# Performance work log

Hardware: AMD Instinct MI355X
Metric: run time of the kernel (lower is better)

The kernel has to match this reference:

```python
import jax, jax.numpy as jnp
import numpy as np

NH, NL, NP_ = 8, 4, 4  # heads, levels, sampling points per head per level
SPATIAL_SHAPES = [(128, 128), (64, 64), (32, 32), (16, 16)]  # (H, W) per level
LIN = sum(h * w for h, w in SPATIAL_SHAPES)  # 21760


def _layernorm(x, g, b, eps=1e-5):
    m = x.mean(-1, keepdims=True)
    v = ((x - m) ** 2).mean(-1, keepdims=True)
    return (x - m) * jax.lax.rsqrt(v + eps) * g + b


def _sample_level(v, H, W, loc):
    # v: [B, NH, H*W, DH] level feature map; loc: [B, Lq, NH, NP, 2] in [0,1]
    # torch grid_sample semantics: align_corners=False, padding_mode='zeros'
    x = loc[..., 0] * W - 0.5
    y = loc[..., 1] * H - 0.5
    x0 = jnp.floor(x); y0 = jnp.floor(y)
    wx = x - x0; wy = y - y0
    x0i = x0.astype(jnp.int32); y0i = y0.astype(jnp.int32)

    def gat(xi, yi):
        valid = (xi >= 0) & (xi < W) & (yi >= 0) & (yi < H)
        idx = jnp.clip(yi, 0, H - 1) * W + jnp.clip(xi, 0, W - 1)  # [B,Lq,NH,NP]
        B_, Lq, nh, P = idx.shape
        idx_t = idx.transpose(0, 2, 1, 3).reshape(B_, nh, Lq * P)
        g = jnp.take_along_axis(v, idx_t[..., None], axis=2)  # [B,NH,Lq*P,DH]
        g = g.reshape(B_, nh, Lq, P, -1).transpose(0, 2, 1, 3, 4)  # [B,Lq,NH,P,DH]
        return g * valid[..., None]

    return (gat(x0i, y0i) * ((1 - wx) * (1 - wy))[..., None]
            + gat(x0i + 1, y0i) * (wx * (1 - wy))[..., None]
            + gat(x0i, y0i + 1) * ((1 - wx) * wy)[..., None]
            + gat(x0i + 1, y0i + 1) * (wx * wy)[..., None])


def _msda(query, ref, src, off_w, off_b, attw_w, attw_b, val_w, val_b, mout_w, mout_b):
    B, Lq, C = query.shape
    DH = C // NH
    value = (src @ val_w.T + val_b).reshape(B, -1, NH, DH).transpose(0, 2, 1, 3)  # [B,NH,Lin,DH]
    offs = (query @ off_w.T + off_b).reshape(B, Lq, NH, NL, NP_, 2)
    aw = jax.nn.softmax((query @ attw_w.T + attw_b).reshape(B, Lq, NH, NL * NP_), axis=-1)
    aw = aw.reshape(B, Lq, NH, NL, NP_)
    # offset normalizer is (W, H) per level
    norm = jnp.array([[w, h] for (h, w) in SPATIAL_SHAPES], jnp.float32)
    loc = ref[:, :, None, :, None, :] + offs / norm[None, None, None, :, None, :]
    out = jnp.zeros((B, Lq, NH, DH), query.dtype)
    start = 0
    for l, (H, W) in enumerate(SPATIAL_SHAPES):
        v_l = value[:, :, start:start + H * W, :]
        start += H * W
        s = _sample_level(v_l, H, W, loc[:, :, :, l])  # [B,Lq,NH,NP,DH]
        out = out + jnp.einsum('bqhpd,bqhp->bqhd', s, aw[:, :, :, l, :])
    return out.reshape(B, Lq, C) @ mout_w.T + mout_b


def _forward(tgt, query_pos, reference_points, src,
             inproj_w, inproj_b, outproj_w, outproj_b,
             ln_inter_g, ln_inter_b, ln_cross_g, ln_cross_b, ln3_g, ln3_b,
             off_w, off_b, attw_w, attw_b, val_w, val_b, mout_w, mout_b,
             lin1_w, lin1_b, lin2_w, lin2_b):
    B, Q, P, C = tgt.shape
    DH = C // NH
    # ---- inter (self) attention over instance axis Q, batched over B*P ----
    x = tgt.swapaxes(1, 2).reshape(B * P, Q, C)
    qkv = x @ inproj_w.T + inproj_b
    q, k, v = jnp.split(qkv, 3, axis=-1)
    q = q.reshape(B * P, Q, NH, DH)
    k = k.reshape(B * P, Q, NH, DH)
    v = v.reshape(B * P, Q, NH, DH)
    att = jax.nn.softmax(jnp.einsum('nqhd,nkhd->nhqk', q, k) / np.float32(np.sqrt(DH)), axis=-1)
    o = jnp.einsum('nhqk,nkhd->nqhd', att, v).reshape(B * P, Q, C) @ outproj_w.T + outproj_b
    x = _layernorm((x + o).reshape(B, P, Q, C), ln_inter_g, ln_inter_b).swapaxes(1, 2)  # [B,Q,P,C]
    # ---- multi-scale deformable cross-attention ----
    query = (x + query_pos).reshape(B, Q * P, C)
    ref = reference_points.reshape(B, Q * P, NL, 2)
    t2 = _msda(query, ref, src, off_w, off_b, attw_w, attw_b, val_w, val_b, mout_w, mout_b).reshape(B, Q, P, C)
    x = _layernorm(x + t2, ln_cross_g, ln_cross_b)
    # ---- FFN ----
    h = jax.nn.relu(x @ lin1_w.T + lin1_b)
    return _layernorm(x + h @ lin2_w.T + lin2_b, ln3_g, ln3_b)


def setup_inputs() -> dict:
    key = jax.random.key(0)
    ks = jax.random.split(key, 24)
    B, Q, P, C, DFF = 4, 300, 16, 256, 1024
    f = jax.random.normal
    w = lambda k, shape: f(k, shape, jnp.float32) * 0.02
    starts = np.cumsum([0] + [h * ww for h, ww in SPATIAL_SHAPES])[:-1]
    return {
        'tgt': f(ks[0], (B, Q, P, C), jnp.float32),
        'query_pos': f(ks[1], (B, Q, P, C), jnp.float32) * 0.1,
        'reference_points': jax.random.uniform(ks[2], (B, Q, P, NL, 2), jnp.float32),
        'src': f(ks[3], (B, LIN, C), jnp.float32),
        'src_spatial_shapes': jnp.array(SPATIAL_SHAPES, jnp.int32),
        'level_start_index': jnp.array(starts, jnp.int32),
        'inproj_w': w(ks[4], (3 * C, C)), 'inproj_b': jnp.zeros((3 * C,), jnp.float32),
        'outproj_w': w(ks[5], (C, C)), 'outproj_b': jnp.zeros((C,), jnp.float32),
        'ln_inter_g': jnp.ones((C,), jnp.float32), 'ln_inter_b': jnp.zeros((C,), jnp.float32),
        'ln_cross_g': jnp.ones((C,), jnp.float32), 'ln_cross_b': jnp.zeros((C,), jnp.float32),
        'ln3_g': jnp.ones((C,), jnp.float32), 'ln3_b': jnp.zeros((C,), jnp.float32),
        'off_w': w(ks[6], (NH * NL * NP_ * 2, C)), 'off_b': jnp.zeros((NH * NL * NP_ * 2,), jnp.float32),
        'attw_w': w(ks[7], (NH * NL * NP_, C)), 'attw_b': jnp.zeros((NH * NL * NP_,), jnp.float32),
        'val_w': w(ks[8], (C, C)), 'val_b': jnp.zeros((C,), jnp.float32),
        'mout_w': w(ks[9], (C, C)), 'mout_b': jnp.zeros((C,), jnp.float32),
        'lin1_w': w(ks[10], (DFF, C)), 'lin1_b': jnp.zeros((DFF,), jnp.float32),
        'lin2_w': w(ks[11], (C, DFF)), 'lin2_b': jnp.zeros((C,), jnp.float32),
    }


def reference(tgt, query_pos, reference_points, src, src_spatial_shapes, level_start_index,
              inproj_w, inproj_b, outproj_w, outproj_b,
              ln_inter_g, ln_inter_b, ln_cross_g, ln_cross_b, ln3_g, ln3_b,
              off_w, off_b, attw_w, attw_b, val_w, val_b, mout_w, mout_b,
              lin1_w, lin1_b, lin2_w, lin2_b):
    # spatial shapes / level starts are compile-time constants (SPATIAL_SHAPES)
    return _forward(tgt, query_pos, reference_points, src,
                    inproj_w, inproj_b, outproj_w, outproj_b,
                    ln_inter_g, ln_inter_b, ln_cross_g, ln_cross_b, ln3_g, ln3_b,
                    off_w, off_b, attw_w, attw_b, val_w, val_b, mout_w, mout_b,
                    lin1_w, lin1_b, lin2_w, lin2_b)
```

## Files before the change

### kernel.cpp

```cpp
#include <hip/hip_runtime.h>
#include <cstdint>
#include <cstddef>

#define B_DIM 4
#define Q_DIM 300
#define P_DIM 16
#define C_DIM 256
#define NHD 8
#define DH 32
#define LQ (Q_DIM*P_DIM)
#define NROW (B_DIM*LQ)
#define LIN_TOT 21760
#define DFF 1024

typedef __attribute__((ext_vector_type(8))) short s16x8;
typedef __attribute__((ext_vector_type(4))) float f32x4;

__device__ __forceinline__ unsigned short f2bf(float f) {
    unsigned u = __float_as_uint(f);
    u = u + 0x7FFFu + ((u >> 16) & 1u);
    return (unsigned short)(u >> 16);
}
__device__ __forceinline__ float bf2f(unsigned short s) {
    return __uint_as_float(((unsigned)s) << 16);
}

template<int RELU, int OBF16, int ABF16, int ADDA>
__global__ __launch_bounds__(256) void gemm_mfma(
    const void* __restrict__ Av, const float* __restrict__ A2,
    const float* __restrict__ W, const float* __restrict__ bias,
    void* __restrict__ Cv, int M, int N, int K)
{
    __shared__ unsigned short As[128 * 72];
    __shared__ unsigned short Ws[64 * 72];
    const int tid = threadIdx.x;
    const int bm = blockIdx.y * 128;
    const int bn = blockIdx.x * 64;
    const int ar = tid >> 1;
    const int ac = (tid & 1) * 32;
    const int wr = tid >> 2;
    const int wc = (tid & 3) * 16;
    const float* Af = (const float*)Av;
    const unsigned short* Ab = (const unsigned short*)Av;
    const float* Afp = Af + (size_t)(bm + ar) * K + ac;
    const unsigned short* Abp = Ab + (size_t)(bm + ar) * K + ac;
    const float* A2p = A2 ? (A2 + (size_t)(bm + ar) * K + ac) : nullptr;
    const float* Wp  = W + (size_t)(bn + wr) * K + wc;
    const int lane = tid & 63;
    const int wid  = tid >> 6;
    const int wm = wid >> 1, wn = wid & 1;
    const int fr = lane & 15;
    const int fq = lane >> 4;
    f32x4 acc[4][2];
    #pragma unroll
    for (int m = 0; m < 4; m++)
        #pragma unroll
        for (int n = 0; n < 2; n++)
            acc[m][n] = (f32x4){0.f, 0.f, 0.f, 0.f};

    for (int k0 = 0; k0 < K; k0 += 64) {
        __syncthreads();
        if (ABF16) {
            #pragma unroll
            for (int j = 0; j < 4; j++)
                *(uint4*)&As[ar*72 + ac + j*8] = *(const uint4*)(Abp + k0 + j*8);
        } else {
            #pragma unroll
            for (int j = 0; j < 4; j++) {
                float4 x = *(const float4*)(Afp + k0 + j*8);
                float4 y = *(const float4*)(Afp + k0 + j*8 + 4);
                if (ADDA) {
                    float4 u = *(const float4*)(A2p + k0 + j*8);
                    float4 v = *(const float4*)(A2p + k0 + j*8 + 4);
                    x.x += u.x; x.y += u.y; x.z += u.z; x.w += u.w;
                    y.x += v.x; y.y += v.y; y.z += v.z; y.w += v.w;
                }
                union { unsigned short s[8]; uint4 v; } pk;
                pk.s[0]=f2bf(x.x); pk.s[1]=f2bf(x.y); pk.s[2]=f2bf(x.z); pk.s[3]=f2bf(x.w);
                pk.s[4]=f2bf(y.x); pk.s[5]=f2bf(y.y); pk.s[6]=f2bf(y.z); pk.s[7]=f2bf(y.w);
                *(uint4*)&As[ar*72 + ac + j*8] = pk.v;
            }
        }
        #pragma unroll
        for (int j = 0; j < 2; j++) {
            float4 x = *(const float4*)(Wp + k0 + j*8);
            float4 y = *(const float4*)(Wp + k0 + j*8 + 4);
            union { unsigned short s[8]; uint4 v; } pk;
            pk.s[0]=f2bf(x.x); pk.s[1]=f2bf(x.y); pk.s[2]=f2bf(x.z); pk.s[3]=f2bf(x.w);
            pk.s[4]=f2bf(y.x); pk.s[5]=f2bf(y.y); pk.s[6]=f2bf(y.z); pk.s[7]=f2bf(y.w);
            *(uint4*)&Ws[wr*72 + wc + j*8] = pk.v;
        }
        __syncthreads();
        #pragma unroll
        for (int ks = 0; ks < 64; ks += 32) {
            s16x8 a0 = *(const s16x8*)&As[(wm*64 +  0 + fr)*72 + ks + fq*8];
            s16x8 a1 = *(const s16x8*)&As[(wm*64 + 16 + fr)*72 + ks + fq*8];
            s16x8 a2 = *(const s16x8*)&As[(wm*64 + 32 + fr)*72 + ks + fq*8];
            s16x8 a3 = *(const s16x8*)&As[(wm*64 + 48 + fr)*72 + ks + fq*8];
            s16x8 b0 = *(const s16x8*)&Ws[(wn*32 +  0 + fr)*72 + ks + fq*8];
            s16x8 b1 = *(const s16x8*)&Ws[(wn*32 + 16 + fr)*72 + ks + fq*8];
            acc[0][0] = __builtin_amdgcn_mfma_f32_16x16x32_bf16(a0, b0, acc[0][0], 0, 0, 0);
            acc[0][1] = __builtin_amdgcn_mfma_f32_16x16x32_bf16(a0, b1, acc[0][1], 0, 0, 0);
            acc[1][0] = __builtin_amdgcn_mfma_f32_16x16x32_bf16(a1, b0, acc[1][0], 0, 0, 0);
            acc[1][1] = __builtin_amdgcn_mfma_f32_16x16x32_bf16(a1, b1, acc[1][1], 0, 0, 0);
            acc[2][0] = __builtin_amdgcn_mfma_f32_16x16x32_bf16(a2, b0, acc[2][0], 0, 0, 0);
            acc[2][1] = __builtin_amdgcn_mfma_f32_16x16x32_bf16(a2, b1, acc[2][1], 0, 0, 0);
            acc[3][0] = __builtin_amdgcn_mfma_f32_16x16x32_bf16(a3, b0, acc[3][0], 0, 0, 0);
            acc[3][1] = __builtin_amdgcn_mfma_f32_16x16x32_bf16(a3, b1, acc[3][1], 0, 0, 0);
        }
    }
    float* Co = (float*)Cv;
    unsigned short* Cb = (unsigned short*)Cv;
    #pragma unroll
    for (int m = 0; m < 4; m++) {
        const int r0 = bm + wm*64 + m*16 + fq*4;
        #pragma unroll
        for (int n = 0; n < 2; n++) {
            const int col = bn + wn*32 + n*16 + fr;
            const float bsv = bias[col];
            #pragma unroll
            for (int j = 0; j < 4; j++) {
                float v = acc[m][n][j] + bsv;
                if (RELU) v = fmaxf(v, 0.f);
                if (OBF16) Cb[(size_t)(r0 + j) * N + col] = f2bf(v);
                else       Co[(size_t)(r0 + j) * N + col] = v;
            }
        }
    }
}

#define KS_ST 40
#define VT_ST 328
#define PB_ST 40
__global__ __launch_bounds__(256) void attn_mfma(
    const unsigned short* __restrict__ qkv, unsigned short* __restrict__ o)
{
    const int h  = blockIdx.x & 7;
    const int bp = blockIdx.x >> 3;
    const int p  = bp & 15;
    const int b  = bp >> 4;
    __shared__ unsigned short Ks[304 * KS_ST];
    __shared__ unsigned short Vt[32 * VT_ST];
    __shared__ unsigned short Pb[4][16 * PB_ST];
    const int tid = threadIdx.x;
    const size_t qbase = ((size_t)b * 4800 + p) * 768 + h * 32;
    for (int k = tid; k < 304; k += 256) {
        uint4 v0, v1, v2, v3;
        if (k < 300) {
            const unsigned short* src = qkv + qbase + (size_t)k * (16*768) + 256;
            v0 = *(const uint4*)(src);      v1 = *(const uint4*)(src + 8);
            v2 = *(const uint4*)(src + 16); v3 = *(const uint4*)(src + 24);
        } else {
            v0 = v1 = v2 = v3 = make_uint4(0u, 0u, 0u, 0u);
        }
        *(uint4*)&Ks[k*KS_ST +  0] = v0; *(uint4*)&Ks[k*KS_ST +  8] = v1;
        *(uint4*)&Ks[k*KS_ST + 16] = v2; *(uint4*)&Ks[k*KS_ST + 24] = v3;
    }
    for (int k = tid; k < 320; k += 256) {
        union { uint4 v[4]; unsigned short s[32]; } t;
        if (k < 300) {
            const unsigned short* src = qkv + qbase + (size_t)k * (16*768) + 512;
            t.v[0] = *(const uint4*)(src);      t.v[1] = *(const uint4*)(src + 8);
            t.v[2] = *(const uint4*)(src + 16); t.v[3] = *(const uint4*)(src + 24);
        } else {
            t.v[0] = t.v[1] = t.v[2] = t.v[3] = make_uint4(0u, 0u, 0u, 0u);
        }
        #pragma unroll
        for (int d = 0; d < 32; d++) Vt[d*VT_ST + k] = t.s[d];
    }
    __syncthreads();

    const int wid = tid >> 6, lane = tid & 63;
    const int fr = lane & 15, fq = lane >> 4;
    const float scale = 0.17677669529663689f;
    unsigned short* Pw = &Pb[wid][0];

    for (int qt = wid; qt < 19; qt += 4) {
        int qr = qt*16 + fr; if (qr > 299) qr = 299;
        const s16x8 aq = *(const s16x8*)(qkv + qbase + (size_t)qr * (16*768) + fq*8);
        f32x4 s[19];
        #pragma unroll
        for (int t = 0; t < 19; t++) {
            s16x8 bk = *(const s16x8*)&Ks[(t*16 + fr)*KS_ST + fq*8];
            s[t] = __builtin_amdgcn_mfma_f32_16x16x32_bf16(aq, bk, (f32x4){0.f,0.f,0.f,0.f}, 0, 0, 0);
        }
        if (fr >= 12) s[18] = (f32x4){-1e30f, -1e30f, -1e30f, -1e30f};
        float mx[4], l[4];
        #pragma unroll
        for (int j = 0; j < 4; j++) {
            float m = s[0][j];
            #pragma unroll
            for (int t = 1; t < 19; t++) m = fmaxf(m, s[t][j]);
            #pragma unroll
            for (int msk = 1; msk < 16; msk <<= 1) m = fmaxf(m, __shfl_xor(m, msk));
            mx[j] = m;
        }
        #pragma unroll
        for (int j = 0; j < 4; j++) {
            float sum = 0.f;
            #pragma unroll
            for (int t = 0; t < 19; t++) {
                const float e = __expf((s[t][j] - mx[j]) * scale);
                s[t][j] = e;
                sum += e;
            }
            #pragma unroll
            for (int msk = 1; msk < 16; msk <<= 1) sum += __shfl_xor(sum, msk);
            l[j] = sum;
        }
        f32x4 oa0 = (f32x4){0.f,0.f,0.f,0.f}, oa1 = (f32x4){0.f,0.f,0.f,0.f};
        #pragma unroll
        for (int st = 0; st < 10; st++) {
            #pragma unroll
            for (int j = 0; j < 4; j++) {
                Pw[(fq*4 + j)*PB_ST + fr]      = f2bf(s[2*st][j]);
                Pw[(fq*4 + j)*PB_ST + 16 + fr] = (2*st + 1 < 19) ? f2bf(s[2*st+1][j])
                                                                 : (unsigned short)0;
            }
            const s16x8 ap = *(const s16x8*)&Pw[fr*PB_ST + fq*8];
            const s16x8 b0 = *(const s16x8*)&Vt[fr*VT_ST + st*32 + fq*8];
            const s16x8 b1 = *(const s16x8*)&Vt[(16 + fr)*VT_ST + st*32 + fq*8];
            oa0 = __builtin_amdgcn_mfma_f32_16x16x32_bf16(ap, b0, oa0, 0, 0, 0);
            oa1 = __builtin_amdgcn_mfma_f32_16x16x32_bf16(ap, b1, oa1, 0, 0, 0);
        }
        #pragma unroll
        for (int j = 0; j < 4; j++) {
            const int q = qt*16 + fq*4 + j;
            if (q < 300) {
                const float inv = 1.0f / l[j];
                unsigned short* op = o + ((size_t)(b*4800 + q*16 + p))*256 + h*32;
                op[fr]      = f2bf(oa0[j] * inv);
                op[16 + fr] = f2bf(oa1[j] * inv);
            }
        }
    }
}

__global__ __launch_bounds__(256) void ln_add_kernel(
    const float* __restrict__ a, const float* __restrict__ b2,
    const float* __restrict__ g, const float* __restrict__ be,
    float* __restrict__ out)
{
    const int row = blockIdx.x;
    const int c = threadIdx.x;
    const size_t idx = (size_t)row * 256 + c;
    const float x = a[idx] + b2[idx];
    float s = x, s2 = x * x;
    #pragma unroll
    for (int m = 32; m >= 1; m >>= 1) {
        s  += __shfl_xor(s, m);
        s2 += __shfl_xor(s2, m);
    }
    __shared__ float ws1[4], ws2[4];
    const int w = threadIdx.x >> 6;
    if ((threadIdx.x & 63) == 0) { ws1[w] = s; ws2[w] = s2; }
    __syncthreads();
    s  = ws1[0] + ws1[1] + ws1[2] + ws1[3];
    s2 = ws2[0] + ws2[1] + ws2[2] + ws2[3];
    const float mean = s * (1.f/256.f);
    const float var  = s2 * (1.f/256.f) - mean * mean;
    const float r = rsqrtf(var + 1e-5f);
    out[idx] = (x - mean) * r * g[c] + be[c];
}

__global__ __launch_bounds__(256) void msda_kernel(
    const unsigned short* __restrict__ value,
    const float* __restrict__ offsattw,
    const float* __restrict__ refp,
    unsigned short* __restrict__ samp)
{
    const int task = blockIdx.x * 4 + (threadIdx.x >> 6);
    const int row = task >> 3;
    const int h   = task & 7;
    const int l   = threadIdx.x & 63;
    const int s   = l >> 2;
    const int cq  = l & 3;

    const float* base = offsattw + (size_t)row * 384;
    const float lg = base[256 + h*16 + s];
    float mxv = lg;
    #pragma unroll
    for (int m = 4; m < 64; m <<= 1) mxv = fmaxf(mxv, __shfl_xor(mxv, m));
    const float e = __expf(lg - mxv);
    float ssum = e;
    #pragma unroll
    for (int m = 4; m < 64; m <<= 1) ssum += __shfl_xor(ssum, m);
    const float w_att = e * (1.0f / ssum);
    const int lv = s >> 2;
    const int Wtab[4]  = {128, 64, 32, 16};
    const int STtab[4] = {0, 16384, 20480, 21504};
    const int W = Wtab[lv];
    const float fW = (float)W;
    const float ox = base[h*32 + s*2];
    const float oy = base[h*32 + s*2 + 1];
    const float rx = refp[(size_t)row*8 + lv*2];
    const float ry = refp[(size_t)row*8 + lv*2 + 1];
    const float x = (rx + ox / fW) * fW - 0.5f;
    const float y = (ry + oy / fW) * fW - 0.5f;
    const float x0f = floorf(x), y0f = floorf(y);
    const float wx = x - x0f, wy = y - y0f;
    const int xi = (int)x0f + (cq & 1);
    const int yi = (int)y0f + (cq >> 1);
    const bool valid = (xi >= 0) & (xi < W) & (yi >= 0) & (yi < W);
    const int xc = min(max(xi, 0), W - 1);
    const int yc = min(max(yi, 0), W - 1);
    const float wxs = (cq & 1)  ? wx : 1.f - wx;
    const float wys = (cq >> 1) ? wy : 1.f - wy;
    const float wgt = valid ? (w_att * wxs * wys) : 0.f;
    const unsigned boff = (unsigned)(STtab[lv] + yc * W + xc) * 512u + (unsigned)h * 64u;

    const char* vb = (const char*)(value + (size_t)(row / LQ) * LIN_TOT * 256);
    float acc[8] = {0.f, 0.f, 0.f, 0.f, 0.f, 0.f, 0.f, 0.f};
    #pragma unroll
    for (int g = 0; g < 4; g++) {
        const int src = g * 16 + s;
        const unsigned a = (unsigned)__shfl((int)boff, src);
        const float    w = __shfl(wgt, src);
        const uint4 v4 = *(const uint4*)(vb + a + cq * 16);
        const unsigned u[4] = {v4.x, v4.y, v4.z, v4.w};
        #pragma unroll
        for (int j = 0; j < 4; j++) {
            acc[2*j]   += w * __uint_as_float(u[j] << 16);
            acc[2*j+1] += w * __uint_as_float(u[j] & 0xFFFF0000u);
        }
    }
    #pragma unroll
    for (int m = 4; m < 64; m <<= 1)
        #pragma unroll
        for (int j = 0; j < 8; j++)
            acc[j] += __shfl_xor(acc[j], m);
    if (s == 0) {
        union { unsigned short sh[8]; uint4 v; } pk;
        #pragma unroll
        for (int j = 0; j < 8; j++) pk.sh[j] = f2bf(acc[j]);
        *(uint4*)(samp + (size_t)row * 256 + h * 32 + cq * 8) = pk.v;
    }
}

extern "C" void kernel_launch(void* const* d_in, const int* in_sizes, int n_in,
                              void* d_out, int out_size, void* d_ws, size_t ws_size,
                              hipStream_t stream)
{
    const float* tgt        = (const float*)d_in[0];
    const float* query_pos  = (const float*)d_in[1];
    const float* refp       = (const float*)d_in[2];
    const float* src        = (const float*)d_in[3];
    const float* inproj_w   = (const float*)d_in[6];
    const float* inproj_b   = (const float*)d_in[7];
    const float* outproj_w  = (const float*)d_in[8];
    const float* outproj_b  = (const float*)d_in[9];
    const float* ln_inter_g = (const float*)d_in[10];
    const float* ln_inter_b = (const float*)d_in[11];
    const float* ln_cross_g = (const float*)d_in[12];
    const float* ln_cross_b = (const float*)d_in[13];
    const float* ln3_g      = (const float*)d_in[14];
    const float* ln3_b      = (const float*)d_in[15];
    const float* off_w      = (const float*)d_in[16];
    const float* off_b      = (const float*)d_in[17];
    const float* attw_w     = (const float*)d_in[18];
    const float* attw_b     = (const float*)d_in[19];
    const float* val_w      = (const float*)d_in[20];
    const float* val_b      = (const float*)d_in[21];
    const float* mout_w     = (const float*)d_in[22];
    const float* mout_b     = (const float*)d_in[23];
    const float* lin1_w     = (const float*)d_in[24];
    const float* lin1_b     = (const float*)d_in[25];
    const float* lin2_w     = (const float*)d_in[26];
    const float* lin2_b     = (const float*)d_in[27];

    float* ws = (float*)d_ws;
    unsigned short* qkv   = (unsigned short*)ws;
    unsigned short* value = (unsigned short*)ws;
    unsigned short* hbuf  = (unsigned short*)ws;
    unsigned short* o1    = (unsigned short*)(ws + 22282240);
    unsigned short* samp  = o1;
    float* f2      = ws + 22282240;
    float* o2      = ws + 27197440;
    float* t2      = o2;
    float* x1      = ws + 32112640;
    float* offsattw= ws + 37027840;
    float* Wm      = ws + 44400640;
    float* Wb      = Wm + 98304;
    float* x2      = ws + 44400640;
    float* outp    = (float*)d_out;

    hipMemcpyAsync(Wm,          off_w,  65536u * 4, hipMemcpyDeviceToDevice, stream);
    hipMemcpyAsync(Wm + 65536,  attw_w, 32768u * 4, hipMemcpyDeviceToDevice, stream);
    hipMemcpyAsync(Wb,          off_b,  256u * 4,   hipMemcpyDeviceToDevice, stream);
    hipMemcpyAsync(Wb + 256,    attw_b, 128u * 4,   hipMemcpyDeviceToDevice, stream);

    gemm_mfma<0,1,0,0><<<dim3(12,150), 256, 0, stream>>>(tgt, nullptr, inproj_w, inproj_b, qkv, NROW, 768, 256);
    attn_mfma<<<512, 256, 0, stream>>>(qkv, o1);
    gemm_mfma<0,0,1,0><<<dim3(4,150), 256, 0, stream>>>(o1, nullptr, outproj_w, outproj_b, o2, NROW, 256, 256);
    ln_add_kernel<<<NROW, 256, 0, stream>>>(tgt, o2, ln_inter_g, ln_inter_b, x1);
    gemm_mfma<0,0,0,1><<<dim3(6,150), 256, 0, stream>>>(x1, query_pos, Wm, Wb, offsattw, NROW, 384, 256);
    gemm_mfma<0,1,0,0><<<dim3(4,680), 256, 0, stream>>>(src, nullptr, val_w, val_b, value, B_DIM * LIN_TOT, 256, 256);
    msda_kernel<<<38400, 256, 0, stream>>>(value, offsattw, refp, samp);
    gemm_mfma<0,0,1,0><<<dim3(4,150), 256, 0, stream>>>(samp, nullptr, mout_w, mout_b, t2, NROW, 256, 256);
    ln_add_kernel<<<NROW, 256, 0, stream>>>(x1, t2, ln_cross_g, ln_cross_b, x2);
    gemm_mfma<1,1,0,0><<<dim3(16,150), 256, 0, stream>>>(x2, nullptr, lin1_w, lin1_b, hbuf, NROW, DFF, 256);
    gemm_mfma<0,0,1,0><<<dim3(4,150), 256, 0, stream>>>(hbuf, nullptr, lin2_w, lin2_b, f2, NROW, 256, DFF);
    ln_add_kernel<<<NROW, 256, 0, stream>>>(x2, f2, ln3_g, ln3_b, outp);
}
```

Before: 632.7 us.

## Pre-cast weights and activations to bf16, add 128x128 GEMM tiles, fuse query_pos add into LayerNorm

All weight matrices are cast to bf16 once per call in a single batched kernel, and tgt is cast once, so the GEMMs no longer convert fp32 weights to bf16 inside every tile. A new 128x128-tile GEMM handles the wide GEMMs (in-proj, offset/attention, value, lin1) to improve operand reuse. The LayerNorm kernels now also emit a bf16 copy, with query_pos added where needed, so the downstream GEMMs read bf16 directly. The costs are extra cast launches and buffers, and higher register use in the larger tile.

```diff
diff --git a/kernel.cpp b/kernel.cpp
--- a/kernel.cpp
+++ b/kernel.cpp
@@ -21,15 +21,124 @@
     u = u + 0x7FFFu + ((u >> 16) & 1u);
     return (unsigned short)(u >> 16);
 }
-__device__ __forceinline__ float bf2f(unsigned short s) {
-    return __uint_as_float(((unsigned)s) << 16);
-}
-
-template<int RELU, int OBF16, int ABF16, int ADDA>
-__global__ __launch_bounds__(256) void gemm_mfma(
-    const void* __restrict__ Av, const float* __restrict__ A2,
-    const float* __restrict__ W, const float* __restrict__ bias,
-    void* __restrict__ Cv, int M, int N, int K)
+
+__global__ __launch_bounds__(256) void cast_bf16(
+    const float* __restrict__ s, unsigned short* __restrict__ d, int n8)
+{
+    const int i = blockIdx.x * 256 + threadIdx.x;
+    if (i < n8) {
+        const float4 x = *(const float4*)(s + (size_t)i*8);
+        const float4 y = *(const float4*)(s + (size_t)i*8 + 4);
+        union { unsigned short sh[8]; uint4 v; } pk;
+        pk.sh[0]=f2bf(x.x); pk.sh[1]=f2bf(x.y); pk.sh[2]=f2bf(x.z); pk.sh[3]=f2bf(x.w);
+        pk.sh[4]=f2bf(y.x); pk.sh[5]=f2bf(y.y); pk.sh[6]=f2bf(y.z); pk.sh[7]=f2bf(y.w);
+        *(uint4*)(d + (size_t)i*8) = pk.v;
+    }
+}
+
+struct W8   { const float* s; unsigned short* d; int n8; };
+struct W8x8 { W8 w[8]; };
+__global__ __launch_bounds__(256) void cast_w8(W8x8 p)
+{
+    const W8 w = p.w[blockIdx.y];
+    for (int i = blockIdx.x * 256 + threadIdx.x; i < w.n8; i += gridDim.x * 256) {
+        const float4 x = *(const float4*)(w.s + (size_t)i*8);
+        const float4 y = *(const float4*)(w.s + (size_t)i*8 + 4);
+        union { unsigned short sh[8]; uint4 v; } pk;
+        pk.sh[0]=f2bf(x.x); pk.sh[1]=f2bf(x.y); pk.sh[2]=f2bf(x.z); pk.sh[3]=f2bf(x.w);
+        pk.sh[4]=f2bf(y.x); pk.sh[5]=f2bf(y.y); pk.sh[6]=f2bf(y.z); pk.sh[7]=f2bf(y.w);
+        *(uint4*)(w.d + (size_t)i*8) = pk.v;
+    }
+}
+
+template<int RELU, int OBF16, int AFP32>
+__global__ __launch_bounds__(256) void gemm_bf16_128(
+    const void* __restrict__ Av, const unsigned short* __restrict__ W,
+    const float* __restrict__ bias, void* __restrict__ Cv, int M, int N, int K)
+{
+    __shared__ unsigned short As[128 * 72];
+    __shared__ unsigned short Ws[128 * 72];
+    const int tid = threadIdx.x;
+    const int bm = blockIdx.y * 128;
+    const int bn = blockIdx.x * 128;
+    const int r  = tid >> 1;
+    const int c  = (tid & 1) * 32;
+    const unsigned short* Ab = (const unsigned short*)Av + (size_t)(bm + r) * K + c;
+    const float*          Af = (const float*)Av          + (size_t)(bm + r) * K + c;
+    const unsigned short* Wp = W + (size_t)(bn + r) * K + c;
+    const int lane = tid & 63;
+    const int wid  = tid >> 6;
+    const int wm = wid >> 1, wn = wid & 1;
+    const int fr = lane & 15;
+    const int fq = lane >> 4;
+    f32x4 acc[4][4];
+    #pragma unroll
+    for (int m = 0; m < 4; m++)
+        #pragma unroll
+        for (int n = 0; n < 4; n++)
+            acc[m][n] = (f32x4){0.f, 0.f, 0.f, 0.f};
+
+    for (int k0 = 0; k0 < K; k0 += 64) {
+        __syncthreads();
+        if (AFP32) {
+            #pragma unroll
+            for (int j = 0; j < 4; j++) {
+                const float4 x = *(const float4*)(Af + k0 + j*8);
+                const float4 y = *(const float4*)(Af + k0 + j*8 + 4);
+                union { unsigned short sh[8]; uint4 v; } pk;
+                pk.sh[0]=f2bf(x.x); pk.sh[1]=f2bf(x.y); pk.sh[2]=f2bf(x.z); pk.sh[3]=f2bf(x.w);
+                pk.sh[4]=f2bf(y.x); pk.sh[5]=f2bf(y.y); pk.sh[6]=f2bf(y.z); pk.sh[7]=f2bf(y.w);
+                *(uint4*)&As[r*72 + c + j*8] = pk.v;
+                *(uint4*)&Ws[r*72 + c + j*8] = *(const uint4*)(Wp + k0 + j*8);
+            }
+        } else {
+            #pragma unroll
+            for (int j = 0; j < 4; j++) {
+                *(uint4*)&As[r*72 + c + j*8] = *(const uint4*)(Ab + k0 + j*8);
+                *(uint4*)&Ws[r*72 + c + j*8] = *(const uint4*)(Wp + k0 + j*8);
+            }
+        }
+        __syncthreads();
+        #pragma unroll
+        for (int ks = 0; ks < 64; ks += 32) {
+            s16x8 a[4], b[4];
+            #pragma unroll
+            for (int m = 0; m < 4; m++)
+                a[m] = *(const s16x8*)&As[(wm*64 + m*16 + fr)*72 + ks + fq*8];
+            #pragma unroll
+            for (int n = 0; n < 4; n++)
+                b[n] = *(const s16x8*)&Ws[(wn*64 + n*16 + fr)*72 + ks + fq*8];
+            #pragma unroll
+            for (int m = 0; m < 4; m++)
+                #pragma unroll
+                for (int n = 0; n < 4; n++)
+                    acc[m][n] = __builtin_amdgcn_mfma_f32_16x16x32_bf16(a[m], b[n], acc[m][n], 0, 0, 0);
+        }
+    }
+    float* Co = (float*)Cv;
+    unsigned short* Cb = (unsigned short*)Cv;
+    #pragma unroll
+    for (int m = 0; m < 4; m++) {
+        const int r0 = bm + wm*64 + m*16 + fq*4;
+        #pragma unroll
+        for (int n = 0; n < 4; n++) {
+            const int col = bn + wn*64 + n*16 + fr;
+            const float bsv = bias[col];
+            #pragma unroll
+            for (int j = 0; j < 4; j++) {
+                float v = acc[m][n][j] + bsv;
+                if (RELU) v = fmaxf(v, 0.f);
+                if (OBF16) Cb[(size_t)(r0 + j) * N + col] = f2bf(v);
+                else       Co[(size_t)(r0 + j) * N + col] = v;
+            }
+        }
+    }
+}
+
+template<int RELU, int OBF16>
+__global__ __launch_bounds__(256) void gemm_bf16_64(
+    const unsigned short* __restrict__ A, const unsigned short* __restrict__ W,
+    const float* __restrict__ bias, void* __restrict__ Cv, int M, int N, int K)
 {
     __shared__ unsigned short As[128 * 72];
     __shared__ unsigned short Ws[64 * 72];
@@ -40,12 +149,8 @@
     const int ac = (tid & 1) * 32;
     const int wr = tid >> 2;
     const int wc = (tid & 3) * 16;
-    const float* Af = (const float*)Av;
-    const unsigned short* Ab = (const unsigned short*)Av;
-    const float* Afp = Af + (size_t)(bm + ar) * K + ac;
-    const unsigned short* Abp = Ab + (size_t)(bm + ar) * K + ac;
-    const float* A2p = A2 ? (A2 + (size_t)(bm + ar) * K + ac) : nullptr;
-    const float* Wp  = W + (size_t)(bn + wr) * K + wc;
+    const unsigned short* Ap = A + (size_t)(bm + ar) * K + ac;
+    const unsigned short* Wp = W + (size_t)(bn + wr) * K + wc;
     const int lane = tid & 63;
     const int wid  = tid >> 6;
     const int wm = wid >> 1, wn = wid & 1;
@@ -60,36 +165,12 @@
 
     for (int k0 = 0; k0 < K; k0 += 64) {
         __syncthreads();
-        if (ABF16) {
-            #pragma unroll
-            for (int j = 0; j < 4; j++)
-                *(uint4*)&As[ar*72 + ac + j*8] = *(const uint4*)(Abp + k0 + j*8);
-        } else {
-            #pragma unroll
-            for (int j = 0; j < 4; j++) {
-                float4 x = *(const float4*)(Afp + k0 + j*8);
-                float4 y = *(const float4*)(Afp + k0 + j*8 + 4);
-                if (ADDA) {
-                    float4 u = *(const float4*)(A2p + k0 + j*8);
-                    float4 v = *(const float4*)(A2p + k0 + j*8 + 4);
-                    x.x += u.x; x.y += u.y; x.z += u.z; x.w += u.w;
-                    y.x += v.x; y.y += v.y; y.z += v.z; y.w += v.w;
-                }
-                union { unsigned short s[8]; uint4 v; } pk;
-                pk.s[0]=f2bf(x.x); pk.s[1]=f2bf(x.y); pk.s[2]=f2bf(x.z); pk.s[3]=f2bf(x.w);
-                pk.s[4]=f2bf(y.x); pk.s[5]=f2bf(y.y); pk.s[6]=f2bf(y.z); pk.s[7]=f2bf(y.w);
-                *(uint4*)&As[ar*72 + ac + j*8] = pk.v;
-            }
-        }
-        #pragma unroll
-        for (int j = 0; j < 2; j++) {
-            float4 x = *(const float4*)(Wp + k0 + j*8);
-            float4 y = *(const float4*)(Wp + k0 + j*8 + 4);
-            union { unsigned short s[8]; uint4 v; } pk;
-            pk.s[0]=f2bf(x.x); pk.s[1]=f2bf(x.y); pk.s[2]=f2bf(x.z); pk.s[3]=f2bf(x.w);
-            pk.s[4]=f2bf(y.x); pk.s[5]=f2bf(y.y); pk.s[6]=f2bf(y.z); pk.s[7]=f2bf(y.w);
-            *(uint4*)&Ws[wr*72 + wc + j*8] = pk.v;
-        }
+        #pragma unroll
+        for (int j = 0; j < 4; j++)
+            *(uint4*)&As[ar*72 + ac + j*8] = *(const uint4*)(Ap + k0 + j*8);
+        #pragma unroll
+        for (int j = 0; j < 2; j++)
+            *(uint4*)&Ws[wr*72 + wc + j*8] = *(const uint4*)(Wp + k0 + j*8);
         __syncthreads();
         #pragma unroll
         for (int ks = 0; ks < 64; ks += 32) {
@@ -236,10 +317,12 @@
     }
 }
 
+template<int EMIT, int HAS_QP>
 __global__ __launch_bounds__(256) void ln_add_kernel(
     const float* __restrict__ a, const float* __restrict__ b2,
     const float* __restrict__ g, const float* __restrict__ be,
-    float* __restrict__ out)
+    const float* __restrict__ qp,
+    float* __restrict__ out, unsigned short* __restrict__ outb)
 {
     const int row = blockIdx.x;
     const int c = threadIdx.x;
@@ -260,7 +343,12 @@
     const float mean = s * (1.f/256.f);
     const float var  = s2 * (1.f/256.f) - mean * mean;
     const float r = rsqrtf(var + 1e-5f);
-    out[idx] = (x - mean) * r * g[c] + be[c];
+    const float y = (x - mean) * r * g[c] + be[c];
+    out[idx] = y;
+    if (EMIT) {
+        const float z = HAS_QP ? y + qp[idx] : y;
+        outb[idx] = f2bf(z);
+    }
 }
 
 __global__ __launch_bounds__(256) void msda_kernel(
@@ -372,33 +460,54 @@
     unsigned short* qkv   = (unsigned short*)ws;
     unsigned short* value = (unsigned short*)ws;
     unsigned short* hbuf  = (unsigned short*)ws;
-    unsigned short* o1    = (unsigned short*)(ws + 22282240);
+    unsigned short* o1    = (unsigned short*)(ws + 11141120);
     unsigned short* samp  = o1;
-    float* f2      = ws + 22282240;
-    float* o2      = ws + 27197440;
+    float* f2      = ws + 11141120;
+    float* o2      = ws + 16056320;
     float* t2      = o2;
-    float* x1      = ws + 32112640;
-    float* offsattw= ws + 37027840;
-    float* Wm      = ws + 44400640;
-    float* Wb      = Wm + 98304;
-    float* x2      = ws + 44400640;
+    float* x1      = ws + 20971520;
+    float* offsattw= ws + 25886720;
+    float* x2      = ws + 33259520;
+    unsigned short* xq   = (unsigned short*)(ws + 38174720);
+    unsigned short* x2b  = (unsigned short*)(ws + 40632320);
+    unsigned short* tgtb = (unsigned short*)(ws + 43089920);
+    unsigned short* wb   = (unsigned short*)(ws + 45547520);
+    unsigned short* wb_inproj = wb;
+    unsigned short* wb_outproj= wb + 196608;
+    unsigned short* wb_m      = wb + 262144;
+    unsigned short* wb_val    = wb + 360448;
+    unsigned short* wb_mout   = wb + 425984;
+    unsigned short* wb_lin1   = wb + 491520;
+    unsigned short* wb_lin2   = wb + 753664;
+    float* Wb      = ws + 46055424;
     float* outp    = (float*)d_out;
 
-    hipMemcpyAsync(Wm,          off_w,  65536u * 4, hipMemcpyDeviceToDevice, stream);
-    hipMemcpyAsync(Wm + 65536,  attw_w, 32768u * 4, hipMemcpyDeviceToDevice, stream);
-    hipMemcpyAsync(Wb,          off_b,  256u * 4,   hipMemcpyDeviceToDevice, stream);
-    hipMemcpyAsync(Wb + 256,    attw_b, 128u * 4,   hipMemcpyDeviceToDevice, stream);
-
-    gemm_mfma<0,1,0,0><<<dim3(12,150), 256, 0, stream>>>(tgt, nullptr, inproj_w, inproj_b, qkv, NROW, 768, 256);
+    {
+        W8x8 p;
+        p.w[0] = { inproj_w,  wb_inproj,  196608/8 };
+        p.w[1] = { outproj_w, wb_outproj,  65536/8 };
+        p.w[2] = { off_w,     wb_m,        65536/8 };
+        p.w[3] = { attw_w,    wb_m+65536,  32768/8 };
+        p.w[4] = { val_w,     wb_val,      65536/8 };
+        p.w[5] = { mout_w,    wb_mout,     65536/8 };
+        p.w[6] = { lin1_w,    wb_lin1,    262144/8 };
+        p.w[7] = { lin2_w,    wb_lin2,    262144/8 };
+        cast_w8<<<dim3(32, 8), 256, 0, stream>>>(p);
+    }
+    cast_bf16<<<2400, 256, 0, stream>>>(tgt, tgtb, 4915200/8);
+    hipMemcpyAsync(Wb,       off_b,  256u * 4, hipMemcpyDeviceToDevice, stream);
+    hipMemcpyAsync(Wb + 256, attw_b, 128u * 4, hipMemcpyDeviceToDevice, stream);
+
+    gemm_bf16_128<0,1,0><<<dim3(6,150), 256, 0, stream>>>(tgtb, wb_inproj, inproj_b, qkv, NROW, 768, 256);
     attn_mfma<<<512, 256, 0, stream>>>(qkv, o1);
-    gemm_mfma<0,0,1,0><<<dim3(4,150), 256, 0, stream>>>(o1, nullptr, outproj_w, outproj_b, o2, NROW, 256, 256);
-    ln_add_kernel<<<NROW, 256, 0, stream>>>(tgt, o2, ln_inter_g, ln_inter_b, x1);
-    gemm_mfma<0,0,0,1><<<dim3(6,150), 256, 0, stream>>>(x1, query_pos, Wm, Wb, offsattw, NROW, 384, 256);
-    gemm_mfma<0,1,0,0><<<dim3(4,680), 256, 0, stream>>>(src, nullptr, val_w, val_b, value, B_DIM * LIN_TOT, 256, 256);
+    gemm_bf16_64<0,0><<<dim3(4,150), 256, 0, stream>>>(o1, wb_outproj, outproj_b, o2, NROW, 256, 256);
+    ln_add_kernel<1,1><<<NROW, 256, 0, stream>>>(tgt, o2, ln_inter_g, ln_inter_b, query_pos, x1, xq);
+    gemm_bf16_128<0,0,0><<<dim3(3,150), 256, 0, stream>>>(xq, wb_m, Wb, offsattw, NROW, 384, 256);
+    gemm_bf16_128<0,1,1><<<dim3(2,680), 256, 0, stream>>>(src, wb_val, val_b, value, B_DIM * LIN_TOT, 256, 256);
     msda_kernel<<<38400, 256, 0, stream>>>(value, offsattw, refp, samp);
-    gemm_mfma<0,0,1,0><<<dim3(4,150), 256, 0, stream>>>(samp, nullptr, mout_w, mout_b, t2, NROW, 256, 256);
-    ln_add_kernel<<<NROW, 256, 0, stream>>>(x1, t2, ln_cross_g, ln_cross_b, x2);
-    gemm_mfma<1,1,0,0><<<dim3(16,150), 256, 0, stream>>>(x2, nullptr, lin1_w, lin1_b, hbuf, NROW, DFF, 256);
-    gemm_mfma<0,0,1,0><<<dim3(4,150), 256, 0, stream>>>(hbuf, nullptr, lin2_w, lin2_b, f2, NROW, 256, DFF);
-    ln_add_kernel<<<NROW, 256, 0, stream>>>(x2, f2, ln3_g, ln3_b, outp);
-}
+    gemm_bf16_64<0,0><<<dim3(4,150), 256, 0, stream>>>(samp, wb_mout, mout_b, t2, NROW, 256, 256);
+    ln_add_kernel<1,0><<<NROW, 256, 0, stream>>>(x1, t2, ln_cross_g, ln_cross_b, nullptr, x2, x2b);
+    gemm_bf16_128<1,1,0><<<dim3(8,150), 256, 0, stream>>>(x2b, wb_lin1, lin1_b, hbuf, NROW, DFF, 256);
+    gemm_bf16_64<0,0><<<dim3(4,150), 256, 0, stream>>>(hbuf, wb_lin2, lin2_b, f2, NROW, 256, DFF);
+    ln_add_kernel<0,0><<<NROW, 256, 0, stream>>>(x2, f2, ln3_g, ln3_b, nullptr, outp, nullptr);
+}
```

Result: faster. 517.1 us (-18.3%).
